# Performance work log

Hardware: AMD Instinct MI355X
Metric: run time of the kernel (lower is better)

## Reference

```python
import jax, jax.numpy as jnp
import numpy as np

IN_F = 4096
OUT_F = 11008
GROUP = 128
GCOUNT = IN_F // GROUP      # 32
PACKS = IN_F // 8           # 512
TOKENS = 4096


def _pack_int4(nibbles):
    # nibbles: (..., K) int32 in [0,16) -> packed (..., K//8) int32
    shifts = jnp.arange(0, 32, 4, dtype=jnp.int32)
    r = nibbles.reshape(*nibbles.shape[:-1], nibbles.shape[-1] // 8, 8)
    return jnp.sum(r << shifts, axis=-1, dtype=jnp.int32)


def setup_inputs() -> dict:
    key = jax.random.key(0)
    k1, k2, k3, k4 = jax.random.split(key, 4)
    x = jax.random.normal(k1, (TOKENS, IN_F), dtype=jnp.float32)
    # generate int4 nibbles then pack along in_features (prepared AWQ layout: (O, K//8))
    nib = jax.random.randint(k2, (OUT_F, IN_F), 0, 16, dtype=jnp.int32)
    qweight = _pack_int4(nib)                              # (O, PACKS) int32
    qzeros = jax.random.randint(k3, (GCOUNT, OUT_F), 0, 16, dtype=jnp.int32)
    scales = (jax.random.uniform(k4, (GCOUNT, OUT_F), dtype=jnp.float32) * 0.02 + 0.001)
    return {"x": x, "qweight": qweight, "qzeros": qzeros, "scales": scales}


def _unpack_int4(packed):
    # packed: (O, K//8) int32 -> (O, K) int32 nibbles
    shifts = jnp.arange(0, 32, 4, dtype=jnp.int32)
    nib = (packed[:, :, None] >> shifts) & 15
    return nib.reshape(packed.shape[0], packed.shape[1] * 8)


def reference(x, qweight, qzeros, scales):
    # group-wise dequant: W[o,k] = (q[o,k] - zero[g,o]) * scale[g,o], g = k // GROUP
    nib = _unpack_int4(qweight).reshape(OUT_F, GCOUNT, GROUP)   # (O, Gc, G)
    z = qzeros.T[:, :, None].astype(jnp.float32)                # (O, Gc, 1)
    s = scales.T[:, :, None]                                    # (O, Gc, 1)
    W = ((nib.astype(jnp.float32) - z) * s).reshape(OUT_F, IN_F)
    # y = x @ W^T
    return jnp.einsum('tk,ok->to', x, W)
```

## Files before the change

### kernel.cpp

```cpp
#include <hip/hip_runtime.h>
#include <hip/hip_bf16.h>
#include <stdint.h>

#define TOKENS 4096
#define IN_F   4096
#define OUT_F  11008
#define PACKS  512
#define GCOUNT 32

#define BM 256
#define BN 256
#define BK 128
#define NKT (IN_F / BK)

typedef __attribute__((ext_vector_type(8))) short bf16x8;
typedef __attribute__((ext_vector_type(4))) float f32x4;
typedef __attribute__((ext_vector_type(4))) int i32x4;

#define AS1 __attribute__((address_space(1)))
#define AS3 __attribute__((address_space(3)))

static __device__ __forceinline__ short f2bf(float f) {
    union { __hip_bfloat16 h; short s; } u;
    u.h = __float2bfloat16(f);
    return u.s;
}

__global__ __launch_bounds__(256) void quant_x_kernel(const float* __restrict__ x,
                                                      signed char* __restrict__ xq,
                                                      float* __restrict__ sx) {
    const int row = blockIdx.x;
    const int t = threadIdx.x;
    const float4* src = (const float4*)(x + (size_t)row * IN_F);
    float4 v[4];
    float am = 0.0f;
#pragma unroll
    for (int i = 0; i < 4; ++i) {
        v[i] = src[t + 256 * i];
        am = fmaxf(am, fmaxf(fmaxf(fabsf(v[i].x), fabsf(v[i].y)),
                             fmaxf(fabsf(v[i].z), fabsf(v[i].w))));
    }
#pragma unroll
    for (int off = 32; off >= 1; off >>= 1)
        am = fmaxf(am, __shfl_xor(am, off));
    __shared__ float wmax[4];
    if ((t & 63) == 0) wmax[t >> 6] = am;
    __syncthreads();
    float amax = fmaxf(fmaxf(wmax[0], wmax[1]), fmaxf(wmax[2], wmax[3]));
    amax = fmaxf(amax, 1e-20f);
    const float rs = 127.0f / amax;
    int* dst = (int*)(xq + (size_t)row * IN_F);
#pragma unroll
    for (int i = 0; i < 4; ++i) {
        float fv[4] = {v[i].x, v[i].y, v[i].z, v[i].w};
        int p = 0;
#pragma unroll
        for (int j = 0; j < 4; ++j) {
            int q = __float2int_rn(fv[j] * rs);
            q = max(-127, min(127, q));
            p |= (q & 255) << (8 * j);
        }
        dst[t + 256 * i] = p;
    }
    if (t == 0) sx[row] = amax * (1.0f / 127.0f);
}

__global__ __launch_bounds__(256) void sw_kernel(const int* __restrict__ qz,
                                                 const float* __restrict__ sc,
                                                 float* __restrict__ sw,
                                                 float* __restrict__ rw) {
    int o = blockIdx.x * 256 + threadIdx.x;
    float wmax = 0.f;
#pragma unroll 8
    for (int g = 0; g < GCOUNT; ++g) {
        float s = sc[(size_t)g * OUT_F + o];
        int z = qz[(size_t)g * OUT_F + o];
        float m = (float)max(z, 15 - z);
        wmax = fmaxf(wmax, s * m);
    }
    sw[o] = wmax * (1.0f / 127.0f);
    rw[o] = 127.0f / wmax;
}

__global__ __launch_bounds__(256) void quant_w8_kernel(const int* __restrict__ qw,
                                                       const int* __restrict__ qz,
                                                       const float* __restrict__ sc,
                                                       const float* __restrict__ rw,
                                                       signed char* __restrict__ wq) {
    int i = blockIdx.x * 256 + threadIdx.x;
    int o = i >> 9, p = i & 511, g = p >> 4;
    int z = qz[(size_t)g * OUT_F + o];
    float f = sc[(size_t)g * OUT_F + o] * rw[o];
    int w = qw[i];
    int lo = 0, hi = 0;
#pragma unroll
    for (int j = 0; j < 4; ++j) {
        int d = __float2int_rn((float)(((w >> (4 * j)) & 15) - z) * f);
        d = max(-127, min(127, d));
        lo |= (d & 255) << (8 * j);
    }
#pragma unroll
    for (int j = 4; j < 8; ++j) {
        int d = __float2int_rn((float)(((w >> (4 * j)) & 15) - z) * f);
        d = max(-127, min(127, d));
        hi |= (d & 255) << (8 * (j - 4));
    }
    ((int2*)wq)[i] = make_int2(lo, hi);
}

__device__ __forceinline__ void stage_i8(const signed char* __restrict__ G, int grow0,
                                         int kt, signed char* lds, int tid) {
#pragma unroll
    for (int i = 0; i < 4; ++i) {
        int CH = i * 512 + tid;
        int r = CH >> 3;
        int c = (CH & 7) ^ (r & 7);
        const signed char* g = G + (size_t)(grow0 + r) * IN_F + kt + c * 16;
        __builtin_amdgcn_global_load_lds((const AS1 void*)g,
                                         (AS3 void*)(lds + CH * 16), 16, 0, 0);
    }
}

#define QUADI(AF, BF, AO, BO)                                                   \
    __builtin_amdgcn_s_setprio(1);                                              \
    _Pragma("unroll") for (int m = 0; m < 4; ++m)                               \
    _Pragma("unroll") for (int n = 0; n < 2; ++n)                               \
    _Pragma("unroll") for (int ks = 0; ks < 2; ++ks)                            \
        iacc[(AO) + m][(BO) + n] = __builtin_amdgcn_mfma_i32_16x16x64_i8(       \
            AF[m][ks], BF[n][ks], iacc[(AO) + m][(BO) + n], 0, 0, 0);           \
    __builtin_amdgcn_s_setprio(0);

__global__ __launch_bounds__(512, 2) void gemm_i8_kernel(const signed char* __restrict__ A,
                                                         const signed char* __restrict__ B,
                                                         const float* __restrict__ sw,
                                                         const float* __restrict__ sx,
                                                         float* __restrict__ C) {
    __shared__ signed char As[2][BM * BK];
    __shared__ signed char Bs[2][BN * BK];

    const int nbn = OUT_F / BN;
    const int nwg = (TOKENS / BM) * nbn;
    const int cpx = nwg >> 3;
    int bid = blockIdx.x;
    int swzb = (bid & 7) * cpx + (bid >> 3);
    int bm = swzb / nbn, bn = swzb % nbn;
    const int row0 = bm * BM, col0 = bn * BN;

    const int tid = threadIdx.x;
    const int lane = tid & 63;
    const int wid = tid >> 6;
    const int wm = wid >> 2, wn = wid & 3;
    const int l15 = lane & 15, lhi = lane >> 4, l7 = lane & 7;
    const int cs0 = ((lhi ^ l7) & 7) * 16;
    const int cs1 = (((4 + lhi) ^ l7) & 7) * 16;
    const int rdA = (wm * 128 + l15) * BK;
    const int rdB = (wn * 64 + l15) * BK;

    i32x4 iacc[8][4] = {};
    i32x4 afA[4][2], afB[4][2], bfA[2][2], bfB[2][2];

    stage_i8(A, row0, 0, &As[0][0], tid);
    stage_i8(B, col0, 0, &Bs[0][0], tid);
    stage_i8(A, row0, BK, &As[1][0], tid);
    asm volatile("s_waitcnt vmcnt(4)" ::: "memory");
    __builtin_amdgcn_s_barrier();

    for (int t = 0; t < NKT; ++t) {
        const int cab = t & 1;
        const signed char* At = &As[cab][0];
        const signed char* Bt = &Bs[cab][0];

#pragma unroll
        for (int m = 0; m < 4; ++m) {
            afA[m][0] = *(const i32x4*)(At + rdA + m * 2048 + cs0);
            afA[m][1] = *(const i32x4*)(At + rdA + m * 2048 + cs1);
        }
        if (t + 1 < NKT) stage_i8(B, col0, (t + 1) * BK, &Bs[cab ^ 1][0], tid);
        __builtin_amdgcn_sched_barrier(0);
        __builtin_amdgcn_s_barrier();
        if (t > 0) { QUADI(afB, bfA, 4, 0); }
        __builtin_amdgcn_s_barrier();

#pragma unroll
        for (int n = 0; n < 2; ++n) {
            bfA[n][0] = *(const i32x4*)(Bt + rdB + n * 2048 + cs0);
            bfA[n][1] = *(const i32x4*)(Bt + rdB + n * 2048 + cs1);
        }
        __builtin_amdgcn_sched_barrier(0);
        __builtin_amdgcn_s_barrier();
        if (t > 0) { QUADI(afB, bfB, 4, 2); }
        __builtin_amdgcn_s_barrier();

#pragma unroll
        for (int m = 0; m < 4; ++m) {
            afB[m][0] = *(const i32x4*)(At + rdA + (4 + m) * 2048 + cs0);
            afB[m][1] = *(const i32x4*)(At + rdA + (4 + m) * 2048 + cs1);
        }
#pragma unroll
        for (int n = 0; n < 2; ++n) {
            bfB[n][0] = *(const i32x4*)(Bt + rdB + (2 + n) * 2048 + cs0);
            bfB[n][1] = *(const i32x4*)(Bt + rdB + (2 + n) * 2048 + cs1);
        }
        __builtin_amdgcn_sched_barrier(0);
        asm volatile("s_waitcnt lgkmcnt(12)" ::: "memory");
        __builtin_amdgcn_sched_barrier(0);
        QUADI(afA, bfA, 0, 0);
        asm volatile("s_waitcnt lgkmcnt(4)" ::: "memory");
        __builtin_amdgcn_sched_barrier(0);
        __builtin_amdgcn_s_barrier();

        if (t + 2 < NKT) stage_i8(A, row0, (t + 2) * BK, &As[cab][0], tid);
        __builtin_amdgcn_sched_barrier(0);
        QUADI(afA, bfB, 0, 2);
        if (t < NKT - 2) {
            asm volatile("s_waitcnt vmcnt(4)" ::: "memory");
        } else if (t == NKT - 2) {
            asm volatile("s_waitcnt vmcnt(0)" ::: "memory");
        }
        __builtin_amdgcn_s_barrier();
    }

    { QUADI(afB, bfA, 4, 0); }
    { QUADI(afB, bfB, 4, 2); }

#pragma unroll
    for (int m = 0; m < 8; ++m) {
        const int rbase = row0 + wm * 128 + m * 16 + lhi * 4;
        f32x4 s4 = *(const f32x4*)(sx + rbase);
#pragma unroll
        for (int n = 0; n < 4; ++n) {
            const int c = col0 + wn * 64 + n * 16 + l15;
            const float swc = sw[c];
#pragma unroll
            for (int j = 0; j < 4; ++j)
                C[(size_t)(rbase + j) * OUT_F + c] = s4[j] * swc * (float)iacc[m][n][j];
        }
    }
}

__device__ __forceinline__ void mfma_tile128(const short* As, const short* Bs,
                                             f32x4 acc[4][4], int lane, int wm, int wn) {
#pragma unroll
    for (int kk = 0; kk < 64; kk += 32) {
        const int kb = kk + (lane >> 4) * 8;
        bf16x8 af[4], bfr[4];
#pragma unroll
        for (int m = 0; m < 4; ++m) {
            int r = wm * 64 + m * 16 + (lane & 15);
            af[m] = *(const bf16x8*)(As + r * 64 + kb);
        }
#pragma unroll
        for (int n = 0; n < 4; ++n) {
            int c = wn * 64 + n * 16 + (lane & 15);
            bfr[n] = *(const bf16x8*)(Bs + c * 64 + kb);
        }
#pragma unroll
        for (int m = 0; m < 4; ++m)
#pragma unroll
            for (int n = 0; n < 4; ++n)
                acc[m][n] = __builtin_amdgcn_mfma_f32_16x16x32_bf16(af[m], bfr[n],
                                                                    acc[m][n], 0, 0, 0);
    }
}

__global__ __launch_bounds__(256) void gemm_fused_kernel(const float* __restrict__ x,
                                                         const int* __restrict__ qw,
                                                         const int* __restrict__ qz,
                                                         const float* __restrict__ sc,
                                                         float* __restrict__ C) {
    const int nbn = OUT_F / 128;
    const int nwg = (TOKENS / 128) * nbn;
    const int cpx = nwg >> 3;
    int bid = blockIdx.x;
    int swzb = (bid & 7) * cpx + (bid >> 3);
    int bm = swzb / nbn, bn = swzb % nbn;
    const int row0 = bm * 128, col0 = bn * 128;

    __shared__ short As[128 * 64];
    __shared__ short Bs[128 * 64];

    const int tid = threadIdx.x;
    const int lane = tid & 63;
    const int wid = tid >> 6;
    const int wm = wid >> 1, wn = wid & 1;

    f32x4 acc[4][4] = {};

    for (int kt = 0; kt < IN_F; kt += 64) {
#pragma unroll
        for (int i = 0; i < 4; ++i) {
            int idx = i * 256 + tid;
            int r = idx >> 3, kc = (idx & 7) * 8;
            const float4* src = (const float4*)(x + (size_t)(row0 + r) * IN_F + kt + kc);
            float4 aa = src[0], bb = src[1];
            bf16x8 v;
            v[0] = f2bf(aa.x); v[1] = f2bf(aa.y); v[2] = f2bf(aa.z); v[3] = f2bf(aa.w);
            v[4] = f2bf(bb.x); v[5] = f2bf(bb.y); v[6] = f2bf(bb.z); v[7] = f2bf(bb.w);
            *(bf16x8*)(As + r * 64 + kc) = v;
        }
        {
            int ol = tid >> 1;
            int kc = (tid & 1) * 32;
            const int4* src = (const int4*)(qw + (size_t)(col0 + ol) * PACKS + ((kt + kc) >> 3));
            int4 w4 = *src;
            int g = kt >> 7;
            float z = (float)qz[(size_t)g * OUT_F + col0 + ol];
            float s = sc[(size_t)g * OUT_F + col0 + ol];
            float zs = z * s;
            const int* wp = (const int*)&w4;
#pragma unroll
            for (int c2 = 0; c2 < 4; ++c2) {
                int w32 = wp[c2];
                bf16x8 v;
#pragma unroll
                for (int j = 0; j < 8; ++j)
                    v[j] = f2bf((float)((w32 >> (4 * j)) & 15) * s - zs);
                *(bf16x8*)(Bs + ol * 64 + kc + c2 * 8) = v;
            }
        }
        __syncthreads();
        mfma_tile128(As, Bs, acc, lane, wm, wn);
        __syncthreads();
    }
#pragma unroll
    for (int m = 0; m < 4; ++m)
#pragma unroll
        for (int n = 0; n < 4; ++n) {
            int r = row0 + wm * 64 + m * 16 + ((lane >> 4) << 2);
            int c = col0 + wn * 64 + n * 16 + (lane & 15);
#pragma unroll
            for (int j = 0; j < 4; ++j)
                C[(size_t)(r + j) * OUT_F + c] = acc[m][n][j];
        }
}

extern "C" void kernel_launch(void* const* d_in, const int* in_sizes, int n_in,
                              void* d_out, int out_size, void* d_ws, size_t ws_size,
                              hipStream_t stream) {
    const float* x = (const float*)d_in[0];
    const int* qw = (const int*)d_in[1];
    const int* qz = (const int*)d_in[2];
    const float* sc = (const float*)d_in[3];
    float* out = (float*)d_out;

    const size_t xq_b = (size_t)TOKENS * IN_F;
    const size_t sx_b = (size_t)TOKENS * 4;
    const size_t sw_b = (size_t)OUT_F * 4;
    const size_t wq_b = (size_t)OUT_F * IN_F;
    const size_t need = xq_b + sx_b + 2 * sw_b + wq_b;

    if (ws_size >= need) {
        signed char* xq = (signed char*)d_ws;
        float* sx = (float*)((char*)d_ws + xq_b);
        float* sw = (float*)((char*)d_ws + xq_b + sx_b);
        float* rw = (float*)((char*)d_ws + xq_b + sx_b + sw_b);
        signed char* wq = (signed char*)((char*)d_ws + xq_b + sx_b + 2 * sw_b);
        quant_x_kernel<<<TOKENS, 256, 0, stream>>>(x, xq, sx);
        sw_kernel<<<OUT_F / 256, 256, 0, stream>>>(qz, sc, sw, rw);
        quant_w8_kernel<<<(OUT_F * PACKS) / 256, 256, 0, stream>>>(qw, qz, sc, rw, wq);
        const int ngemm = (TOKENS / BM) * (OUT_F / BN);
        gemm_i8_kernel<<<ngemm, 512, 0, stream>>>(xq, wq, sw, sx, out);
    } else {
        gemm_fused_kernel<<<(TOKENS / 128) * (OUT_F / 128), 256, 0, stream>>>(x, qw, qz, sc, out);
    }
}
```

Measured before the change: 270.8 us.

## Load B fragments directly from global memory, bypassing LDS staging

The int8 weight tile is no longer staged through shared memory. Each lane now reads its B MFMA fragments straight from global memory into registers, which halves LDS usage and removes several barriers per K step. The block swizzle is also changed to iterate over M within each N column, so neighbouring blocks reuse the same weight columns through L2. The risk is exposing global load latency directly in front of the MFMAs, with little prefetch distance, and less coalesced global access than the staged path.

```diff
diff --git a/kernel.cpp b/kernel.cpp
--- a/kernel.cpp
+++ b/kernel.cpp
@@ -136,14 +136,13 @@
                                                          const float* __restrict__ sx,
                                                          float* __restrict__ C) {
     __shared__ signed char As[2][BM * BK];
-    __shared__ signed char Bs[2][BN * BK];
-
-    const int nbn = OUT_F / BN;
-    const int nwg = (TOKENS / BM) * nbn;
+
+    const int nbm = TOKENS / BM;
+    const int nwg = nbm * (OUT_F / BN);
     const int cpx = nwg >> 3;
     int bid = blockIdx.x;
     int swzb = (bid & 7) * cpx + (bid >> 3);
-    int bm = swzb / nbn, bn = swzb % nbn;
+    int bn = swzb / nbm, bm = swzb % nbm;
     const int row0 = bm * BM, col0 = bn * BN;
 
     const int tid = threadIdx.x;
@@ -154,13 +153,13 @@
     const int cs0 = ((lhi ^ l7) & 7) * 16;
     const int cs1 = (((4 + lhi) ^ l7) & 7) * 16;
     const int rdA = (wm * 128 + l15) * BK;
-    const int rdB = (wn * 64 + l15) * BK;
+
+    const signed char* Bbase = B + (size_t)(col0 + wn * 64 + l15) * IN_F + lhi * 16;
 
     i32x4 iacc[8][4] = {};
     i32x4 afA[4][2], afB[4][2], bfA[2][2], bfB[2][2];
 
     stage_i8(A, row0, 0, &As[0][0], tid);
-    stage_i8(B, col0, 0, &Bs[0][0], tid);
     stage_i8(A, row0, BK, &As[1][0], tid);
     asm volatile("s_waitcnt vmcnt(4)" ::: "memory");
     __builtin_amdgcn_s_barrier();
@@ -168,55 +167,56 @@
     for (int t = 0; t < NKT; ++t) {
         const int cab = t & 1;
         const signed char* At = &As[cab][0];
-        const signed char* Bt = &Bs[cab][0];
+        const size_t kb = (size_t)t * BK;
 
 #pragma unroll
         for (int m = 0; m < 4; ++m) {
             afA[m][0] = *(const i32x4*)(At + rdA + m * 2048 + cs0);
             afA[m][1] = *(const i32x4*)(At + rdA + m * 2048 + cs1);
         }
-        if (t + 1 < NKT) stage_i8(B, col0, (t + 1) * BK, &Bs[cab ^ 1][0], tid);
-        __builtin_amdgcn_sched_barrier(0);
-        __builtin_amdgcn_s_barrier();
+        __builtin_amdgcn_sched_barrier(0);
         if (t > 0) { QUADI(afB, bfA, 4, 0); }
-        __builtin_amdgcn_s_barrier();
-
+        __builtin_amdgcn_sched_barrier(0);
 #pragma unroll
         for (int n = 0; n < 2; ++n) {
-            bfA[n][0] = *(const i32x4*)(Bt + rdB + n * 2048 + cs0);
-            bfA[n][1] = *(const i32x4*)(Bt + rdB + n * 2048 + cs1);
-        }
-        __builtin_amdgcn_sched_barrier(0);
-        __builtin_amdgcn_s_barrier();
+            bfA[n][0] = *(const i32x4*)(Bbase + (size_t)(n * 16) * IN_F + kb);
+            bfA[n][1] = *(const i32x4*)(Bbase + (size_t)(n * 16) * IN_F + kb + 64);
+        }
+        __builtin_amdgcn_sched_barrier(0);
+
         if (t > 0) { QUADI(afB, bfB, 4, 2); }
-        __builtin_amdgcn_s_barrier();
+        __builtin_amdgcn_sched_barrier(0);
+#pragma unroll
+        for (int n = 0; n < 2; ++n) {
+            bfB[n][0] = *(const i32x4*)(Bbase + (size_t)((2 + n) * 16) * IN_F + kb);
+            bfB[n][1] = *(const i32x4*)(Bbase + (size_t)((2 + n) * 16) * IN_F + kb + 64);
+        }
+        __builtin_amdgcn_sched_barrier(0);
 
 #pragma unroll
         for (int m = 0; m < 4; ++m) {
             afB[m][0] = *(const i32x4*)(At + rdA + (4 + m) * 2048 + cs0);
             afB[m][1] = *(const i32x4*)(At + rdA + (4 + m) * 2048 + cs1);
         }
-#pragma unroll
-        for (int n = 0; n < 2; ++n) {
-            bfB[n][0] = *(const i32x4*)(Bt + rdB + (2 + n) * 2048 + cs0);
-            bfB[n][1] = *(const i32x4*)(Bt + rdB + (2 + n) * 2048 + cs1);
-        }
-        __builtin_amdgcn_sched_barrier(0);
-        asm volatile("s_waitcnt lgkmcnt(12)" ::: "memory");
+        __builtin_amdgcn_sched_barrier(0);
+        asm volatile("s_waitcnt lgkmcnt(8)" ::: "memory");
+        asm volatile("s_waitcnt vmcnt(4)" ::: "memory");
         __builtin_amdgcn_sched_barrier(0);
         QUADI(afA, bfA, 0, 0);
-        asm volatile("s_waitcnt lgkmcnt(4)" ::: "memory");
+        asm volatile("s_waitcnt lgkmcnt(0)" ::: "memory");
         __builtin_amdgcn_sched_barrier(0);
         __builtin_amdgcn_s_barrier();
 
         if (t + 2 < NKT) stage_i8(A, row0, (t + 2) * BK, &As[cab][0], tid);
         __builtin_amdgcn_sched_barrier(0);
+        if (t + 2 < NKT) {
+            asm volatile("s_waitcnt vmcnt(4)" ::: "memory");
+        } else {
+            asm volatile("s_waitcnt vmcnt(0)" ::: "memory");
+        }
+        __builtin_amdgcn_sched_barrier(0);
         QUADI(afA, bfB, 0, 2);
-        if (t < NKT - 2) {
-            asm volatile("s_waitcnt vmcnt(4)" ::: "memory");
-        } else if (t == NKT - 2) {
-            asm volatile("s_waitcnt vmcnt(0)" ::: "memory");
-        }
+        __builtin_amdgcn_sched_barrier(0);
         __builtin_amdgcn_s_barrier();
     }
 
```

After: 343.9 us. +27.0%, slower.
